# Optimization experiments

Hardware: AMD Instinct MI355X
Metric: run time of the kernel (lower is better)

## Reference

```python
import jax, jax.numpy as jnp
import numpy as np

STRIDES = (8.0, 16.0, 32.0)
NC, DFL = 80, 16
NO = NC + 4 * DFL            # 144
TOPK, ALPHA, BETA, EPS = 10, 0.5, 6.0, 1e-9
MAXB = 32                    # static max gt boxes per image (pad rows are masked out)
W_CLS, W_BOX, W_DFL = 0.5, 7.5, 1.5
B, IMG, NT = 16, 640, 256


def _make_anchors(shapes, strides, offset=0.5):
    pts, strs = [], []
    for (h, w), s in zip(shapes, strides):
        sx = jnp.arange(w, dtype=jnp.float32) + offset
        sy = jnp.arange(h, dtype=jnp.float32) + offset
        gy, gx = jnp.meshgrid(sy, sx, indexing='ij')
        pts.append(jnp.stack([gx, gy], -1).reshape(-1, 2))
        strs.append(jnp.full((h * w, 1), s, dtype=jnp.float32))
    return jnp.concatenate(pts, 0), jnp.concatenate(strs, 0)


def _ciou(box1, box2, eps=1e-7):
    b1x1, b1y1, b1x2, b1y2 = jnp.split(box1, 4, -1)
    b2x1, b2y1, b2x2, b2y2 = jnp.split(box2, 4, -1)
    w1, h1 = b1x2 - b1x1, b1y2 - b1y1 + eps
    w2, h2 = b2x2 - b2x1, b2y2 - b2y1 + eps
    inter = (jnp.maximum(jnp.minimum(b1x2, b2x2) - jnp.maximum(b1x1, b2x1), 0.0) *
             jnp.maximum(jnp.minimum(b1y2, b2y2) - jnp.maximum(b1y1, b2y1), 0.0))
    union = w1 * h1 + w2 * h2 - inter + eps
    iou = inter / union
    cw = jnp.maximum(b1x2, b2x2) - jnp.minimum(b1x1, b2x1)
    ch = jnp.maximum(b1y2, b2y2) - jnp.minimum(b1y1, b2y1)
    c2 = cw ** 2 + ch ** 2 + eps
    rho2 = ((b2x1 + b2x2 - b1x1 - b1x2) ** 2 + (b2y1 + b2y2 - b1y1 - b1y2) ** 2) / 4
    v = (4.0 / np.pi ** 2) * (jnp.arctan(w2 / h2) - jnp.arctan(w1 / h1)) ** 2
    a = jax.lax.stop_gradient(v / (v - iou + (1.0 + eps)))
    return iou - (rho2 / c2 + v * a)     # [..., 1]


def _assign(scores, bboxes, gt_labels, gt_bboxes, mask_gt, anchors):
    # Task-aligned assigner (YOLOv8 TAL). All inputs are gradient-stopped.
    b, a, c = scores.shape
    n = gt_bboxes.shape[1]
    lt, rb = gt_bboxes[..., :2], gt_bboxes[..., 2:]
    deltas = jnp.concatenate([anchors[None, None] - lt[:, :, None],
                              rb[:, :, None] - anchors[None, None]], -1)        # [b,n,a,4]
    mask_in_gts = (deltas.min(-1) > EPS).astype(scores.dtype)                   # [b,n,a]
    overlaps = jnp.maximum(_ciou(gt_bboxes[:, :, None], bboxes[:, None])[..., 0], 0.0)
    labels = gt_labels[..., 0].astype(jnp.int32)                                # [b,n]
    bbox_scores = jax.vmap(lambda s, l: jnp.take(s, l, axis=1).T)(scores, labels)  # [b,n,a]
    align = bbox_scores ** ALPHA * overlaps ** BETA
    mask_true = mask_in_gts * mask_gt                                           # [b,n,a]
    metrics = align * mask_true
    tkv, tki = jax.lax.top_k(metrics, TOPK)                                     # [b,n,k]
    valid = jnp.max(tkv, -1, keepdims=True) > EPS
    tki = jnp.where(valid, tki, 0)
    bi = jnp.arange(b)[:, None, None]
    ni = jnp.arange(n)[None, :, None]
    cnt = jnp.zeros((b, n, a), scores.dtype).at[bi, ni, tki].add(1.0)
    mask_topk = jnp.where(cnt > 1, 0.0, cnt)
    mask_pos = mask_topk * mask_true
    fg = mask_pos.sum(1)                                                        # [b,a]
    multi = (fg > 1)[:, None, :]
    is_max = jnp.transpose(jax.nn.one_hot(jnp.argmax(overlaps, 1), n, dtype=scores.dtype), (0, 2, 1))
    mask_pos = jnp.where(multi, is_max, mask_pos)
    fg = mask_pos.sum(1)
    tgi = jnp.argmax(mask_pos, 1)                                               # [b,a]
    t_labels = jnp.take_along_axis(labels, tgi, axis=1)
    t_bboxes = jnp.take_along_axis(gt_bboxes, jnp.broadcast_to(tgi[..., None], (b, a, 4)), axis=1)
    t_scores = jax.nn.one_hot(jnp.maximum(t_labels, 0), NC, dtype=scores.dtype) * (fg > 0)[..., None]
    align = align * mask_pos
    pos_align = jnp.max(align, -1, keepdims=True)                               # [b,n,1]
    pos_ovl = jnp.max(overlaps * mask_pos, -1, keepdims=True)
    norm = jnp.max(align * pos_ovl / (pos_align + EPS), 1)[..., None]           # [b,a,1]
    return t_bboxes, t_scores * norm, fg > 0


def _forward(p3, p4, p5, targets):
    x = [jnp.transpose(o, (0, 3, 1, 2)) for o in (p3, p4, p5)]                  # NCHW
    b = x[0].shape[0]
    out = jnp.concatenate([o.reshape(b, NO, -1) for o in x], 2)
    pred_dist = jnp.transpose(out[:, :4 * DFL], (0, 2, 1))                      # [b,A,64]
    pred_scores = jnp.transpose(out[:, 4 * DFL:], (0, 2, 1))                    # [b,A,80]
    shapes = [o.shape[2:4] for o in x]
    size = jnp.array(shapes[0], jnp.float32) * STRIDES[0]                       # [H, W] pixels
    anchor_points, stride_tensor = _make_anchors(shapes, STRIDES)
    # per-image padded gt tensor (vectorized replacement of the TF scatter loop)
    img = targets[:, 0].astype(jnp.int32)
    nt = targets.shape[0]
    pos = jnp.arange(nt)
    rank = jnp.sum((img[None, :] == img[:, None]) & (pos[None, :] < pos[:, None]), 1)
    gt = jnp.zeros((b, MAXB, 5), jnp.float32).at[img, rank].set(targets[:, 1:])
    scale = jnp.stack([size[1], size[0], size[1], size[0]])
    xywh = gt[..., 1:5] * scale
    gt_bboxes = jnp.concatenate([xywh[..., :2] - xywh[..., 2:] / 2,
                                 xywh[..., :2] + xywh[..., 2:] / 2], -1)
    gt_labels = gt[..., 0:1]
    mask_gt = (jnp.sum(gt_bboxes, 2, keepdims=True) > 0).astype(jnp.float32)    # [b,n,1]
    a_num = pred_dist.shape[1]
    project = jnp.arange(DFL, dtype=jnp.float32)
    pd = jax.nn.softmax(pred_dist.reshape(b, a_num, 4, DFL), -1)
    pd = jnp.einsum('bafc,c->baf', pd, project)                                 # DFL expectation
    pred_bboxes = jnp.concatenate([anchor_points - pd[..., :2],
                                   anchor_points + pd[..., 2:]], -1)            # [b,A,4]
    scores = jax.lax.stop_gradient(jax.nn.sigmoid(pred_scores))
    bboxes = jax.lax.stop_gradient(pred_bboxes * stride_tensor)
    t_bboxes, t_scores, fg = _assign(scores, bboxes, gt_labels, gt_bboxes, mask_gt,
                                     anchor_points * stride_tensor)
    t_bboxes = t_bboxes / stride_tensor
    tss = jnp.maximum(jnp.sum(t_scores), 1.0)
    z, l = t_scores, pred_scores
    bce = jnp.maximum(l, 0.0) - l * z + jnp.log1p(jnp.exp(-jnp.abs(l)))
    loss_cls = jnp.sum(bce) / tss
    fgf = fg.astype(jnp.float32)
    weight = jnp.sum(t_scores, -1) * fgf                                        # [b,A], 0 off-fg
    iou = _ciou(pred_bboxes, t_bboxes)[..., 0]
    loss_box = jnp.sum((1.0 - iou) * weight) / tss
    lt_rb = jnp.concatenate([anchor_points - t_bboxes[..., :2],
                             t_bboxes[..., 2:] - anchor_points], -1)
    lt_rb = jnp.clip(lt_rb, 0.0, DFL - 1.01)                                    # [b,A,4]
    logp = jax.nn.log_softmax(pred_dist.reshape(b, a_num, 4, DFL), -1)
    tl = lt_rb.astype(jnp.int32)
    wl = (tl + 1).astype(jnp.float32) - lt_rb
    left = -jnp.take_along_axis(logp, tl[..., None], -1)[..., 0]
    right = -jnp.take_along_axis(logp, (tl + 1)[..., None], -1)[..., 0]
    dfl = jnp.mean(left * wl + right * (1.0 - wl), -1)                          # [b,A]
    loss_dfl = jnp.sum(dfl * weight) / tss
    return W_CLS * loss_cls + W_BOX * loss_box + W_DFL * loss_dfl


def setup_inputs() -> dict:
    key = jax.random.key(0)
    k1, k2, k3, k4, k5, k6 = jax.random.split(key, 6)
    p3 = jax.random.normal(k1, (B, IMG // 8, IMG // 8, NO), jnp.float32)
    p4 = jax.random.normal(k2, (B, IMG // 16, IMG // 16, NO), jnp.float32)
    p5 = jax.random.normal(k3, (B, IMG // 32, IMG // 32, NO), jnp.float32)
    img = (jnp.arange(NT) % B).astype(jnp.float32)        # exactly 16 boxes / image <= MAXB
    cls = jax.random.randint(k4, (NT,), 0, NC).astype(jnp.float32)
    xy = jax.random.uniform(k5, (NT, 2), minval=0.25, maxval=0.75)
    wh = jax.random.uniform(k6, (NT, 2), minval=0.05, maxval=0.30)
    targets = jnp.concatenate([img[:, None], cls[:, None], xy, wh], -1)   # [NT,6]
    return {"p3": p3, "p4": p4, "p5": p5, "targets": targets}


def reference(p3, p4, p5, targets):
    return _forward(p3, p4, p5, targets)
```

## Files before the change

### kernel.cpp

```cpp
#include <hip/hip_runtime.h>
#include <math.h>

#define A_TOT 8400
#define NB 16
#define NG 32
#define NCH 144
#define NDFL 16
#define EPSF 1e-9f
#define CEPS 1e-7f
#define INV_PI2_4 0.40528473456935109f
#define NBLK2 2100
#define LSEG 512
#define K56_BLOCKS 32

#define LOADU(p)  __hip_atomic_load((p), __ATOMIC_ACQUIRE, __HIP_MEMORY_SCOPE_AGENT)
#define LOADF(p)  __hip_atomic_load((p), __ATOMIC_ACQUIRE, __HIP_MEMORY_SCOPE_AGENT)

#define OFF_GTBOX   0
#define OFF_GTLAB   2048
#define OFF_MASKGT  2560
#define OFF_ATANGT  3072
#define OFF_ACC     3584
#define OFF_CTRL    3592
#define OFF_BCNT    3600
#define OFF_PART2   3856
#define OFF_PART6   5968
#define OFF_POSM    6224
#define OFF_PBOX    10320
#define OFF_MPOS    547920
#define OFF_LIST    682320

__device__ __forceinline__ void locate(int a, int& loc, int& W, float& s, int& lvl, int& hw){
  if (a < 6400)      { lvl = 0; loc = a;        W = 80; s = 8.f;  hw = 6400; }
  else if (a < 8000) { lvl = 1; loc = a - 6400; W = 40; s = 16.f; hw = 1600; }
  else               { lvl = 2; loc = a - 8000; W = 20; s = 32.f; hw = 400;  }
}

__device__ __forceinline__ const float* level_ptr(const float* p3, const float* p4, const float* p5, int lvl){
  return lvl == 0 ? p3 : (lvl == 1 ? p4 : p5);
}

__device__ __forceinline__ float ciou_gp(float gx1,float gy1,float gx2,float gy2,float atg,
                                         float px1,float py1,float px2,float py2,float atp){
  float w1 = gx2-gx1, h1 = gy2-gy1+CEPS;
  float w2 = px2-px1, h2 = py2-py1+CEPS;
  float iw = fmaxf(fminf(gx2,px2)-fmaxf(gx1,px1), 0.f);
  float ih = fmaxf(fminf(gy2,py2)-fmaxf(gy1,py1), 0.f);
  float inter = iw*ih;
  float uni = w1*h1 + w2*h2 - inter + CEPS;
  float iou = inter/uni;
  float cw = fmaxf(gx2,px2)-fminf(gx1,px1);
  float ch = fmaxf(gy2,py2)-fminf(gy1,py1);
  float c2 = cw*cw + ch*ch + CEPS;
  float dx = px1+px2-gx1-gx2, dy = py1+py2-gy1-gy2;
  float rho2 = (dx*dx + dy*dy)*0.25f;
  float dv = atp - atg;
  float v = INV_PI2_4*dv*dv;
  float al = v/(v - iou + (1.f + CEPS));
  return iou - (rho2/c2 + v*al);
}

__global__ __launch_bounds__(256) void k2x(const float* __restrict__ p3, const float* __restrict__ p4,
                          const float* __restrict__ p5, const float* __restrict__ tgt, int nt,
                          float* __restrict__ ws){
  int tid = threadIdx.x;
  int bx = blockIdx.x;
  if (bx == NBLK2){
    __shared__ int simg[256];
    float* gtbox  = ws + OFF_GTBOX;
    int*   gtlab  = (int*)(ws + OFF_GTLAB);
    float* maskgt = ws + OFF_MASKGT;
    float* atangt = ws + OFF_ATANGT;
    for (int i = tid; i < NB*NG*4; i += 256) gtbox[i] = 0.f;
    for (int i = tid; i < NB*NG; i += 256) gtlab[i] = 0;
    if (tid < 8){ (ws + OFF_ACC)[tid] = 0.f; ((unsigned*)(ws + OFF_CTRL))[tid] = 0u; }
    for (int i = tid; i < 256;  i += 256) ((unsigned*)(ws + OFF_BCNT))[i] = 0u;
    for (int i = tid; i < NB*NG*8; i += 256) (ws + OFF_POSM)[i] = 0.f;
    for (int i = tid; i < nt && i < 256; i += 256) simg[i] = (int)tgt[i*6];
    __syncthreads();
    for (int i = tid; i < nt && i < 256; i += 256){
      int b = simg[i];
      int r = 0;
      for (int j = 0; j < i; j++) r += (simg[j] == b);
      if (b >= 0 && b < NB && r < NG){
        float cls = tgt[i*6+1];
        float cx = tgt[i*6+2]*640.f, cy = tgt[i*6+3]*640.f;
        float w  = tgt[i*6+4]*640.f, h  = tgt[i*6+5]*640.f;
        int o = (b*NG + r)*4;
        gtbox[o+0] = cx - 0.5f*w; gtbox[o+1] = cy - 0.5f*h;
        gtbox[o+2] = cx + 0.5f*w; gtbox[o+3] = cy + 0.5f*h;
        gtlab[b*NG + r] = (int)cls;
      }
    }
    __syncthreads();
    for (int i = tid; i < NB*NG; i += 256){
      float x1 = gtbox[i*4], y1 = gtbox[i*4+1], x2 = gtbox[i*4+2], y2 = gtbox[i*4+3];
      maskgt[i] = ((x1+y1+x2+y2) > 0.f) ? 1.f : 0.f;
      atangt[i] = atanf((x2-x1)/(y2-y1+CEPS));
    }
    return;
  }
  __shared__ float redw[4];
  {
    int mp = bx*256 + tid;
    if (mp < NB*A_TOT) ((unsigned*)(ws + OFF_MPOS))[mp] = 0u;
  }
  const float* base; int grow0, hw, W, lvloff;
  if (bx < 1600)      { base = p3; grow0 = bx*64;        hw = 6400; W = 80; lvloff = 0; }
  else if (bx < 2000) { base = p4; grow0 = (bx-1600)*64; hw = 1600; W = 40; lvloff = 6400; }
  else                { base = p5; grow0 = (bx-2000)*64; hw = 400;  W = 20; lvloff = 8000; }

  const float4* src = (const float4*)base + (size_t)grow0*36;
  {
    int r = tid >> 2, f = tid & 3;
    const float4* rp = src + r*36 + f*4;
    float4 v0 = rp[0], v1 = rp[1], v2 = rp[2], v3 = rp[3];
    float m = v0.x;
    m = fmaxf(m, v0.y); m = fmaxf(m, v0.z); m = fmaxf(m, v0.w);
    m = fmaxf(m, v1.x); m = fmaxf(m, v1.y); m = fmaxf(m, v1.z); m = fmaxf(m, v1.w);
    m = fmaxf(m, v2.x); m = fmaxf(m, v2.y); m = fmaxf(m, v2.z); m = fmaxf(m, v2.w);
    m = fmaxf(m, v3.x); m = fmaxf(m, v3.y); m = fmaxf(m, v3.z); m = fmaxf(m, v3.w);
    float e, se, swe;
    e = __expf(v0.x - m); se = e;            swe = 0.f;
    e = __expf(v0.y - m); se += e;           swe += e;
    e = __expf(v0.z - m); se += e;           swe = fmaf(2.f,  e, swe);
    e = __expf(v0.w - m); se += e;           swe = fmaf(3.f,  e, swe);
    e = __expf(v1.x - m); se += e;           swe = fmaf(4.f,  e, swe);
    e = __expf(v1.y - m); se += e;           swe = fmaf(5.f,  e, swe);
    e = __expf(v1.z - m); se += e;           swe = fmaf(6.f,  e, swe);
    e = __expf(v1.w - m); se += e;           swe = fmaf(7.f,  e, swe);
    e = __expf(v2.x - m); se += e;           swe = fmaf(8.f,  e, swe);
    e = __expf(v2.y - m); se += e;           swe = fmaf(9.f,  e, swe);
    e = __expf(v2.z - m); se += e;           swe = fmaf(10.f, e, swe);
    e = __expf(v2.w - m); se += e;           swe = fmaf(11.f, e, swe);
    e = __expf(v3.x - m); se += e;           swe = fmaf(12.f, e, swe);
    e = __expf(v3.y - m); se += e;           swe = fmaf(13.f, e, swe);
    e = __expf(v3.z - m); se += e;           swe = fmaf(14.f, e, swe);
    e = __expf(v3.w - m); se += e;           swe = fmaf(15.f, e, swe);
    float pdf = __fdividef(swe, se);
    float s1 = __shfl_xor(pdf, 1);
    float s2 = __shfl_xor(pdf, 2);
    float s3 = __shfl_xor(pdf, 3);
    if (f == 0){
      int grow = grow0 + r;
      int b = grow / hw, loc = grow - b*hw;
      float ax = (loc % W) + 0.5f, ay = (loc / W) + 0.5f;
      float4 pb;
      pb.x = ax - pdf; pb.y = ay - s1; pb.z = ax + s2; pb.w = ay + s3;
      ((float4*)(ws + OFF_PBOX))[(size_t)b*A_TOT + lvloff + loc] = pb;
    }
  }
  float sp = 0.f;
  #pragma unroll
  for (int i = 0; i < 5; i++){
    int id = i*256 + tid;
    int r = id/20, q = id - r*20;
    float4 v = src[r*36 + 16 + q];
    #pragma unroll
    for (int e2 = 0; e2 < 4; e2++){
      float x = (&v.x)[e2];
      float ex = __expf(-fabsf(x));
      sp += fmaxf(x, 0.f) + __logf(1.f + ex);
    }
  }
  #pragma unroll
  for (int st = 1; st < 64; st <<= 1) sp += __shfl_xor(sp, st);
  int wid = tid >> 6, lane = tid & 63;
  if (lane == 0) redw[wid] = sp;
  __syncthreads();
  if (tid == 0) (ws + OFF_PART2)[bx] = redw[0]+redw[1]+redw[2]+redw[3];
}

#define REG_K 15
__global__ __launch_bounds__(512) void k4x(const float* __restrict__ p3, const float* __restrict__ p4,
                        const float* __restrict__ p5, float* __restrict__ ws){
  int tid = threadIdx.x;
  int lane = tid & 63;
  int g = blockIdx.x*8 + (tid >> 6);
  int b = g >> 5, n = g & 31;
  float mk = ws[OFF_MASKGT + b*NG + n];
  if (mk <= 0.f) return;
  int lab = ((const int*)(ws + OFF_GTLAB))[b*NG + n];
  int ch = 64 + lab;
  float atg = ws[OFF_ATANGT + b*NG + n];
  const float* gt = ws + OFF_GTBOX + (b*NG + n)*4;
  float gx1 = gt[0], gy1 = gt[1], gx2 = gt[2], gy2 = gt[3];

  int clo0 = max(0, (int)floorf(gx1*0.125f   - 0.5f));
  int chi0 = min(79,(int)ceilf (gx2*0.125f   - 0.5f));
  int rlo0 = max(0, (int)floorf(gy1*0.125f   - 0.5f));
  int rhi0 = min(79,(int)ceilf (gy2*0.125f   - 0.5f));
  int clo1 = max(0, (int)floorf(gx1*0.0625f  - 0.5f));
  int chi1 = min(39,(int)ceilf (gx2*0.0625f  - 0.5f));
  int rlo1 = max(0, (int)floorf(gy1*0.0625f  - 0.5f));
  int rhi1 = min(39,(int)ceilf (gy2*0.0625f  - 0.5f));
  int clo2 = max(0, (int)floorf(gx1*0.03125f - 0.5f));
  int chi2 = min(19,(int)ceilf (gx2*0.03125f - 0.5f));
  int rlo2 = max(0, (int)floorf(gy1*0.03125f - 0.5f));
  int rhi2 = min(19,(int)ceilf (gy2*0.03125f - 0.5f));
  int nc0 = chi0-clo0+1, nr0 = rhi0-rlo0+1;
  int nc1 = chi1-clo1+1, nr1 = rhi1-rlo1+1;
  int nc2 = chi2-clo2+1, nr2 = rhi2-rlo2+1;
  int cnt0 = (nc0>0 && nr0>0) ? nc0*nr0 : 0;
  int cnt1 = (nc1>0 && nr1>0) ? nc1*nr1 : 0;
  int cnt2 = (nc2>0 && nr2>0) ? nc2*nr2 : 0;
  const int CAP = 64*REG_K;
  if (16+cnt0 > CAP)           cnt0 = CAP-16;
  if (16+cnt0+cnt1 > CAP)      cnt1 = CAP-16-cnt0;
  if (16+cnt0+cnt1+cnt2 > CAP) cnt2 = CAP-16-cnt0-cnt1;
  int b1 = 16 + cnt0, b2 = b1 + cnt1;
  int tot = b2 + cnt2;

  float mv[REG_K]; int mi[REG_K];
  #pragma unroll
  for (int cc = 0; cc < REG_K; cc++){
    mv[cc] = -1e30f; mi[cc] = 0x7fffffff;
    int c = cc*64 + lane;
    if (c < tot){
      int aidx, loc, W, hw; float s; const float* bp; bool dup = false;
      if (c < 16)     { aidx = c; loc = c; W = 80; s = 8.f;  hw = 6400; bp = p3; }
      else if (c < b1){ int j = c-16; int rr = j/nc0; loc = (rlo0+rr)*80 + clo0 + (j - rr*nc0);
                        aidx = loc;        W = 80; s = 8.f;  hw = 6400; bp = p3; dup = (aidx < 16); }
      else if (c < b2){ int j = c-b1; int rr = j/nc1; loc = (rlo1+rr)*40 + clo1 + (j - rr*nc1);
                        aidx = 6400 + loc; W = 40; s = 16.f; hw = 1600; bp = p4; }
      else            { int j = c-b2; int rr = j/nc2; loc = (rlo2+rr)*20 + clo2 + (j - rr*nc2);
                        aidx = 8000 + loc; W = 20; s = 32.f; hw = 400;  bp = p5; }
      if (dup){ mv[cc] = -1.f; mi[cc] = 0x3fffffff; }
      else {
        float m = 0.f;
        float axi = ((loc % W) + 0.5f)*s, ayi = ((loc / W) + 0.5f)*s;
        float dmin = fminf(fminf(axi-gx1, ayi-gy1), fminf(gx2-axi, gy2-ayi));
        if (dmin > EPSF){
          float4 pg = ((const float4*)(ws + OFF_PBOX))[(size_t)b*A_TOT + aidx];
          float px1 = pg.x*s, py1 = pg.y*s, px2 = pg.z*s, py2 = pg.w*s;
          float atp = atanf((px2-px1)/(py2-py1+CEPS));
          float o = fmaxf(ciou_gp(gx1,gy1,gx2,gy2,atg, px1,py1,px2,py2,atp), 0.f);
          float l = bp[((size_t)b*hw + loc)*NCH + ch];
          float sc = __frcp_rn(1.f + __expf(-l));
          float o2 = o*o;
          m = sqrtf(sc)*o2*o2*o2;
        }
        mv[cc] = m; mi[cc] = aidx;
      }
    }
  }
  float top0 = 0.f;
  int mytop = -1;
  #pragma unroll
  for (int k = 0; k < 10; k++){
    float bv = -1e30f; int bai = 0x7fffffff;
    #pragma unroll
    for (int cc = 0; cc < REG_K; cc++){
      if (mv[cc] > bv || (mv[cc] == bv && mi[cc] < bai)){ bv = mv[cc]; bai = mi[cc]; }
    }
    #pragma unroll
    for (int st = 1; st < 64; st <<= 1){
      float ov = __shfl_xor(bv, st);
      int  oai = __shfl_xor(bai, st);
      if (ov > bv || (ov == bv && oai < bai)){ bv = ov; bai = oai; }
    }
    if (k == 0) top0 = bv;
    if (lane == k) mytop = bai;
    #pragma unroll
    for (int cc = 0; cc < REG_K; cc++){
      if (mi[cc] == bai) mv[cc] = -2.f;
    }
  }
  bool want = (lane < 10) && (top0 > EPSF) && (mytop >= 0) && (mytop < A_TOT);
  if (want){
    int loc, W, lvl, hw; float s;
    locate(mytop, loc, W, s, lvl, hw);
    float axi = ((loc % W) + 0.5f)*s, ayi = ((loc / W) + 0.5f)*s;
    float dmin = fminf(fminf(axi-gx1, ayi-gy1), fminf(gx2-axi, gy2-ayi));
    want = (dmin > EPSF);
  }
  unsigned old = 0u;
  if (want) old = atomicOr((unsigned*)(ws + OFF_MPOS) + (size_t)b*A_TOT + mytop, 1u << n);
  want = want && (old == 0u);
  unsigned long long m64 = __ballot(want);
  if (want){
    int lead = __ffsll((long long)m64) - 1;
    unsigned base = 0;
    if (lane == lead) base = atomicAdd((unsigned*)(ws + OFF_BCNT) + b*16, (unsigned)__popcll(m64));
    base = __shfl(base, lead);
    unsigned slot = base + (unsigned)__popcll(m64 & ((1ull << lane) - 1ull));
    if (slot < LSEG) ((unsigned*)(ws + OFF_LIST))[b*LSEG + slot] = (unsigned)mytop;
  }
}

__global__ __launch_bounds__(256) void k56x(const float* __restrict__ p3, const float* __restrict__ p4,
                        const float* __restrict__ p5, float* __restrict__ ws, float* __restrict__ out){
  __shared__ float redw[16];
  __shared__ float fin[4];
  __shared__ int lastf;
  __shared__ unsigned cnt_s;
  int tid = threadIdx.x;
  int lane = tid & 63, wid = tid >> 6;
  int s_id = blockIdx.x*256 + tid;
  int b = s_id >> 9, i = s_id & (LSEG-1);
  if (tid == 0) cnt_s = (b < NB) ? LOADU((unsigned*)(ws + OFF_BCNT) + b*16) : 0u;
  __syncthreads();
  unsigned cntb = cnt_s;
  bool valid = false; int a = 0;
  if (b < NB && (unsigned)i < cntb && cntb <= LSEG){
    valid = true;
    a = (int)((unsigned*)(ws + OFF_LIST))[b*LSEG + i];
  }
  int ns = 0; float av = 0.f;
  int loc=0, W=80, lvl=0, hw=6400; float sfac=8.f;
  if (valid){
    unsigned bits = ((const unsigned*)(ws + OFF_MPOS))[(size_t)b*A_TOT + a];
    locate(a, loc, W, sfac, lvl, hw);
    float4 pg = ((const float4*)(ws + OFF_PBOX))[(size_t)b*A_TOT + a];
    float px1 = pg.x*sfac, py1 = pg.y*sfac, px2 = pg.z*sfac, py2 = pg.w*sfac;
    float atp = atanf((px2-px1)/(py2-py1+CEPS));
    if (__popc(bits) == 1){ ns = __ffs(bits) - 1; }
    else {
      float bv = -1.f; ns = 0;
      for (int nn = 0; nn < NG; nn++){
        const float* g = ws + OFF_GTBOX + (b*NG + nn)*4;
        float atg = ws[OFF_ATANGT + b*NG + nn];
        float o = fmaxf(ciou_gp(g[0],g[1],g[2],g[3],atg, px1,py1,px2,py2,atp), 0.f);
        if (o > bv){ bv = o; ns = nn; }
      }
    }
    const float* g = ws + OFF_GTBOX + (b*NG + ns)*4;
    float atg = ws[OFF_ATANGT + b*NG + ns];
    float o = fmaxf(ciou_gp(g[0],g[1],g[2],g[3],atg, px1,py1,px2,py2,atp), 0.f);
    int lab = ((const int*)(ws + OFF_GTLAB))[b*NG + ns];
    float l = level_ptr(p3,p4,p5,lvl)[((size_t)b*hw + loc)*NCH + 64 + lab];
    float sc = __frcp_rn(1.f + __expf(-l));
    float o2 = o*o;
    av = sqrtf(sc)*o2*o2*o2;
    unsigned* pm = (unsigned*)(ws + OFF_POSM) + (b*NG + ns)*8;
    atomicMax(pm + 0, __float_as_uint(av));
    atomicMax(pm + 1, __float_as_uint(o));
  }
  if (blockIdx.x == 0){
    float v = 0.f;
    for (int j = tid; j < NBLK2; j += 256) v += (ws + OFF_PART2)[j];
    #pragma unroll
    for (int st = 1; st < 64; st <<= 1) v += __shfl_xor(v, st);
    if (lane == 0) redw[wid] = v;
    __syncthreads();
    if (tid == 0)
      __hip_atomic_store(ws + OFF_ACC + 0, redw[0]+redw[1]+redw[2]+redw[3],
                         __ATOMIC_RELEASE, __HIP_MEMORY_SCOPE_AGENT);
    __syncthreads();
  }
  __syncthreads();
  if (tid == 0){
    __threadfence();
    __hip_atomic_fetch_add((unsigned*)(ws + OFF_CTRL) + 1, 1u,
                           __ATOMIC_ACQ_REL, __HIP_MEMORY_SCOPE_AGENT);
    while (LOADU((unsigned*)(ws + OFF_CTRL) + 1) < K56_BLOCKS){ __builtin_amdgcn_s_sleep(1); }
  }
  __syncthreads();
  __threadfence();
  float bcec = 0.f, boxl = 0.f, dfll = 0.f, tsc = 0.f;
  if (valid){
    unsigned* pm = (unsigned*)(ws + OFF_POSM) + (b*NG + ns)*8;
    float pa = __uint_as_float(LOADU(pm + 0));
    float po = __uint_as_float(LOADU(pm + 1));
    float norm = av * po / (pa + EPSF);
    const float* row = level_ptr(p3,p4,p5,lvl) + ((size_t)b*hw + loc)*NCH;
    int lab = ((const int*)(ws + OFF_GTLAB))[b*NG + ns];
    if (lab < 0) lab = 0;
    tsc = norm;
    bcec = -row[64 + lab]*norm;
    float4 pb = ((const float4*)(ws + OFF_PBOX))[(size_t)b*A_TOT + a];
    const float* g = ws + OFF_GTBOX + (b*NG + ns)*4;
    float inv_s = 1.f/sfac;
    float tx1 = g[0]*inv_s, ty1 = g[1]*inv_s, tx2 = g[2]*inv_s, ty2 = g[3]*inv_s;
    float w1 = pb.z-pb.x, h1 = pb.w-pb.y+CEPS;
    float w2 = tx2-tx1,   h2 = ty2-ty1+CEPS;
    float iw = fmaxf(fminf(pb.z,tx2)-fmaxf(pb.x,tx1), 0.f);
    float ih = fmaxf(fminf(pb.w,ty2)-fmaxf(pb.y,ty1), 0.f);
    float inter = iw*ih;
    float uni = w1*h1 + w2*h2 - inter + CEPS;
    float iou = inter/uni;
    float cw = fmaxf(pb.z,tx2)-fminf(pb.x,tx1);
    float ch = fmaxf(pb.w,ty2)-fminf(pb.y,ty1);
    float c2 = cw*cw + ch*ch + CEPS;
    float dx = tx1+tx2-pb.x-pb.z, dy = ty1+ty2-pb.y-pb.w;
    float rho2 = (dx*dx + dy*dy)*0.25f;
    float dv = atanf(w2/h2) - atanf(w1/h1);
    float v = INV_PI2_4*dv*dv;
    float al = v/(v - iou + (1.f + CEPS));
    float ci = iou - (rho2/c2 + v*al);
    boxl = (1.f - ci)*norm;
    float ax = (loc % W) + 0.5f, ay = (loc / W) + 0.5f;
    float ltrb[4] = {ax - tx1, ay - ty1, tx2 - ax, ty2 - ay};
    float ds = 0.f;
    #pragma unroll
    for (int f = 0; f < 4; f++){
      float val = fminf(fmaxf(ltrb[f], 0.f), (float)NDFL - 1.01f);
      int tl = (int)val;
      float wl = (float)(tl + 1) - val;
      float x[16];
      const float4* r4 = (const float4*)(row + f*16);
      #pragma unroll
      for (int q = 0; q < 4; q++){ float4 vv = r4[q]; x[q*4]=vv.x; x[q*4+1]=vv.y; x[q*4+2]=vv.z; x[q*4+3]=vv.w; }
      float m = x[0];
      #pragma unroll
      for (int j = 1; j < 16; j++) m = fmaxf(m, x[j]);
      float se = 0.f;
      #pragma unroll
      for (int j = 0; j < 16; j++) se += __expf(x[j]-m);
      float lse = m + __logf(se);
      float xl = 0.f, xr = 0.f;
      #pragma unroll
      for (int j = 0; j < 16; j++){
        xl = (j == tl)   ? x[j] : xl;
        xr = (j == tl+1) ? x[j] : xr;
      }
      ds += (lse - xl)*wl + (lse - xr)*(1.f - wl);
    }
    dfll = ds*0.25f*norm;
  }
  float vals[4] = {bcec, boxl, dfll, tsc};
  #pragma unroll
  for (int q = 0; q < 4; q++){
    float v = vals[q];
    #pragma unroll
    for (int st = 1; st < 64; st <<= 1) v += __shfl_xor(v, st);
    if (lane == 0) redw[wid*4 + q] = v;
  }
  if (tid == 0) lastf = 0;
  __syncthreads();
  if (tid < 4){
    float v = redw[tid] + redw[4+tid] + redw[8+tid] + redw[12+tid];
    __hip_atomic_store(ws + OFF_PART6 + blockIdx.x*4 + tid, v,
                       __ATOMIC_RELEASE, __HIP_MEMORY_SCOPE_AGENT);
  }
  __syncthreads();
  if (tid == 0){
    __threadfence();
    unsigned tkt = __hip_atomic_fetch_add((unsigned*)(ws + OFF_CTRL) + 2, 1u,
                                          __ATOMIC_ACQ_REL, __HIP_MEMORY_SCOPE_AGENT);
    if (tkt == K56_BLOCKS - 1) lastf = 1;
  }
  __syncthreads();
  if (lastf){
    if (tid < 4) fin[tid] = 0.f;
    __syncthreads();
    if (tid < 4*K56_BLOCKS){
      float v = LOADF(ws + OFF_PART6 + tid);
      atomicAdd(&fin[tid & 3], v);
    }
    __syncthreads();
    if (tid == 0){
      float sp = LOADF(ws + OFF_ACC + 0);
      float tss = fmaxf(fin[3], 1.f);
      out[0] = (0.5f*(sp + fin[0]) + 7.5f*fin[1] + 1.5f*fin[2]) / tss;
    }
  }
}

extern "C" void kernel_launch(void* const* d_in, const int* in_sizes, int n_in,
                              void* d_out, int out_size, void* d_ws, size_t ws_size,
                              hipStream_t stream) {
  const float* p3 = (const float*)d_in[0];
  const float* p4 = (const float*)d_in[1];
  const float* p5 = (const float*)d_in[2];
  const float* tg = (const float*)d_in[3];
  int nt = in_sizes[3] / 6;
  float* ws = (float*)d_ws;
  float* out = (float*)d_out;

  k2x<<<NBLK2 + 1, 256, 0, stream>>>(p3, p4, p5, tg, nt, ws);
  k4x<<<64, 512, 0, stream>>>(p3, p4, p5, ws);
  k56x<<<K56_BLOCKS, 256, 0, stream>>>(p3, p4, p5, ws, out);
}
```

Baseline: 76.72 us.

## Use one 256-thread block per GT box with packed 64-bit top-k keys

The top-k assignment kernel now runs one block of 256 threads per ground-truth box instead of one wavefront per box, so 512 blocks launch instead of 64. Candidate metric and anchor index are packed into a single 64-bit key, which makes the argmax a plain max, and a shared-memory step combines the four wavefront results. Each candidate thread holds at most 4 keys instead of 15, and the candidate cap rises from 960 to 1024. The cost is two block barriers per top-k iteration, and a shift in tie-breaking, since duplicate anchors now carry key 0 rather than a sentinel.

```diff
diff --git a/kernel.cpp b/kernel.cpp
--- a/kernel.cpp
+++ b/kernel.cpp
@@ -12,6 +12,7 @@
 #define NBLK2 2100
 #define LSEG 512
 #define K56_BLOCKS 32
+#define K4CAP 1024
 
 #define LOADU(p)  __hip_atomic_load((p), __ATOMIC_ACQUIRE, __HIP_MEMORY_SCOPE_AGENT)
 #define LOADF(p)  __hip_atomic_load((p), __ATOMIC_ACQUIRE, __HIP_MEMORY_SCOPE_AGENT)
@@ -171,13 +172,13 @@
   if (tid == 0) (ws + OFF_PART2)[bx] = redw[0]+redw[1]+redw[2]+redw[3];
 }
 
-#define REG_K 15
-__global__ __launch_bounds__(512) void k4x(const float* __restrict__ p3, const float* __restrict__ p4,
+__global__ __launch_bounds__(256) void k4x(const float* __restrict__ p3, const float* __restrict__ p4,
                         const float* __restrict__ p5, float* __restrict__ ws){
+  __shared__ unsigned long long wk[4];
   int tid = threadIdx.x;
-  int lane = tid & 63;
-  int g = blockIdx.x*8 + (tid >> 6);
-  int b = g >> 5, n = g & 31;
+  int lane = tid & 63, wid = tid >> 6;
+  int bx = blockIdx.x;
+  int b = bx >> 5, n = bx & 31;
   float mk = ws[OFF_MASKGT + b*NG + n];
   if (mk <= 0.f) return;
   int lab = ((const int*)(ws + OFF_GTLAB))[b*NG + n];
@@ -204,29 +205,27 @@
   int cnt0 = (nc0>0 && nr0>0) ? nc0*nr0 : 0;
   int cnt1 = (nc1>0 && nr1>0) ? nc1*nr1 : 0;
   int cnt2 = (nc2>0 && nr2>0) ? nc2*nr2 : 0;
-  const int CAP = 64*REG_K;
-  if (16+cnt0 > CAP)           cnt0 = CAP-16;
-  if (16+cnt0+cnt1 > CAP)      cnt1 = CAP-16-cnt0;
-  if (16+cnt0+cnt1+cnt2 > CAP) cnt2 = CAP-16-cnt0-cnt1;
+  if (16+cnt0 > K4CAP)           cnt0 = K4CAP-16;
+  if (16+cnt0+cnt1 > K4CAP)      cnt1 = K4CAP-16-cnt0;
+  if (16+cnt0+cnt1+cnt2 > K4CAP) cnt2 = K4CAP-16-cnt0-cnt1;
   int b1 = 16 + cnt0, b2 = b1 + cnt1;
   int tot = b2 + cnt2;
 
-  float mv[REG_K]; int mi[REG_K];
+  unsigned long long key[4];
   #pragma unroll
-  for (int cc = 0; cc < REG_K; cc++){
-    mv[cc] = -1e30f; mi[cc] = 0x7fffffff;
-    int c = cc*64 + lane;
+  for (int j = 0; j < 4; j++){
+    key[j] = 0ull;
+    int c = j*256 + tid;
     if (c < tot){
       int aidx, loc, W, hw; float s; const float* bp; bool dup = false;
       if (c < 16)     { aidx = c; loc = c; W = 80; s = 8.f;  hw = 6400; bp = p3; }
-      else if (c < b1){ int j = c-16; int rr = j/nc0; loc = (rlo0+rr)*80 + clo0 + (j - rr*nc0);
+      else if (c < b1){ int jj = c-16; int rr = jj/nc0; loc = (rlo0+rr)*80 + clo0 + (jj - rr*nc0);
                         aidx = loc;        W = 80; s = 8.f;  hw = 6400; bp = p3; dup = (aidx < 16); }
-      else if (c < b2){ int j = c-b1; int rr = j/nc1; loc = (rlo1+rr)*40 + clo1 + (j - rr*nc1);
+      else if (c < b2){ int jj = c-b1; int rr = jj/nc1; loc = (rlo1+rr)*40 + clo1 + (jj - rr*nc1);
                         aidx = 6400 + loc; W = 40; s = 16.f; hw = 1600; bp = p4; }
-      else            { int j = c-b2; int rr = j/nc2; loc = (rlo2+rr)*20 + clo2 + (j - rr*nc2);
+      else            { int jj = c-b2; int rr = jj/nc2; loc = (rlo2+rr)*20 + clo2 + (jj - rr*nc2);
                         aidx = 8000 + loc; W = 20; s = 32.f; hw = 400;  bp = p5; }
-      if (dup){ mv[cc] = -1.f; mi[cc] = 0x3fffffff; }
-      else {
+      if (!dup){
         float m = 0.f;
         float axi = ((loc % W) + 0.5f)*s, ayi = ((loc / W) + 0.5f)*s;
         float dmin = fminf(fminf(axi-gx1, ayi-gy1), fminf(gx2-axi, gy2-ayi));
@@ -240,33 +239,34 @@
           float o2 = o*o;
           m = sqrtf(sc)*o2*o2*o2;
         }
-        mv[cc] = m; mi[cc] = aidx;
+        key[j] = ((unsigned long long)__float_as_uint(m) << 32)
+               | (unsigned long long)(0xFFFFFFFFu - (unsigned)aidx);
       }
     }
   }
-  float top0 = 0.f;
+  float top0m = 0.f;
   int mytop = -1;
-  #pragma unroll
   for (int k = 0; k < 10; k++){
-    float bv = -1e30f; int bai = 0x7fffffff;
-    #pragma unroll
-    for (int cc = 0; cc < REG_K; cc++){
-      if (mv[cc] > bv || (mv[cc] == bv && mi[cc] < bai)){ bv = mv[cc]; bai = mi[cc]; }
-    }
+    unsigned long long bk = key[0];
+    #pragma unroll
+    for (int j = 1; j < 4; j++) if (key[j] > bk) bk = key[j];
     #pragma unroll
     for (int st = 1; st < 64; st <<= 1){
-      float ov = __shfl_xor(bv, st);
-      int  oai = __shfl_xor(bai, st);
-      if (ov > bv || (ov == bv && oai < bai)){ bv = ov; bai = oai; }
-    }
-    if (k == 0) top0 = bv;
-    if (lane == k) mytop = bai;
-    #pragma unroll
-    for (int cc = 0; cc < REG_K; cc++){
-      if (mi[cc] == bai) mv[cc] = -2.f;
-    }
-  }
-  bool want = (lane < 10) && (top0 > EPSF) && (mytop >= 0) && (mytop < A_TOT);
+      unsigned long long ok = __shfl_xor(bk, st);
+      if (ok > bk) bk = ok;
+    }
+    if (lane == 0) wk[wid] = bk;
+    __syncthreads();
+    unsigned long long fk = wk[0];
+    #pragma unroll
+    for (int w = 1; w < 4; w++) if (wk[w] > fk) fk = wk[w];
+    if (k == 0) top0m = __uint_as_float((unsigned)(fk >> 32));
+    if (tid == k) mytop = (int)(0xFFFFFFFFu - (unsigned)(fk & 0xFFFFFFFFull));
+    #pragma unroll
+    for (int j = 0; j < 4; j++) if (key[j] == fk) key[j] = 0ull;
+    __syncthreads();
+  }
+  bool want = (tid < 64) && (lane < 10) && (top0m > EPSF) && (mytop >= 0) && (mytop < A_TOT);
   if (want){
     int loc, W, lvl, hw; float s;
     locate(mytop, loc, W, s, lvl, hw);
@@ -274,17 +274,19 @@
     float dmin = fminf(fminf(axi-gx1, ayi-gy1), fminf(gx2-axi, gy2-ayi));
     want = (dmin > EPSF);
   }
-  unsigned old = 0u;
-  if (want) old = atomicOr((unsigned*)(ws + OFF_MPOS) + (size_t)b*A_TOT + mytop, 1u << n);
-  want = want && (old == 0u);
-  unsigned long long m64 = __ballot(want);
-  if (want){
-    int lead = __ffsll((long long)m64) - 1;
-    unsigned base = 0;
-    if (lane == lead) base = atomicAdd((unsigned*)(ws + OFF_BCNT) + b*16, (unsigned)__popcll(m64));
-    base = __shfl(base, lead);
-    unsigned slot = base + (unsigned)__popcll(m64 & ((1ull << lane) - 1ull));
-    if (slot < LSEG) ((unsigned*)(ws + OFF_LIST))[b*LSEG + slot] = (unsigned)mytop;
+  if (tid < 64){
+    unsigned old = 0u;
+    if (want) old = atomicOr((unsigned*)(ws + OFF_MPOS) + (size_t)b*A_TOT + mytop, 1u << n);
+    bool w2 = want && (old == 0u);
+    unsigned long long m64 = __ballot(w2);
+    if (w2){
+      int lead = __ffsll((long long)m64) - 1;
+      unsigned base = 0;
+      if (lane == lead) base = atomicAdd((unsigned*)(ws + OFF_BCNT) + b*16, (unsigned)__popcll(m64));
+      base = __shfl(base, lead);
+      unsigned slot = base + (unsigned)__popcll(m64 & ((1ull << lane) - 1ull));
+      if (slot < LSEG) ((unsigned*)(ws + OFF_LIST))[b*LSEG + slot] = (unsigned)mytop;
+    }
   }
 }
 
@@ -469,6 +471,6 @@
   float* out = (float*)d_out;
 
   k2x<<<NBLK2 + 1, 256, 0, stream>>>(p3, p4, p5, tg, nt, ws);
-  k4x<<<64, 512, 0, stream>>>(p3, p4, p5, ws);
+  k4x<<<NB*NG, 256, 0, stream>>>(p3, p4, p5, ws);
   k56x<<<K56_BLOCKS, 256, 0, stream>>>(p3, p4, p5, ws, out);
 }
```

After: 61.74 us. 1.24x faster.
